# Optimization experiments

Measured on AMD Instinct MI355X. Metric: run time of the kernel, lower is better.

## Reference

```python
import jax, jax.numpy as jnp
import numpy as np

R = 1          # box filter radius -> 3x3 kernel
EPS = 0.01     # regularization


def _box_kernel(r, ch):
    k = 2 * r + 1
    return jnp.full((ch, 1, k, k), 1.0 / (k * k), dtype=jnp.float32)


def _box(x, kernel, groups):
    # depthwise box filter, stride 1, 'same' padding (NCHW)
    return jax.lax.conv_general_dilated(
        x, kernel, window_strides=(1, 1), padding='SAME',
        dimension_numbers=('NCHW', 'OIHW', 'NCHW'),
        feature_group_count=groups)


def setup_inputs() -> dict:
    key = jax.random.key(0)
    k1, k2 = jax.random.split(key)
    shape = (8, 3, 1024, 1024)
    return {
        'x': jax.random.normal(k1, shape, dtype=jnp.float32),
        'y': jax.random.normal(k2, shape, dtype=jnp.float32),
    }


def reference(x, y):
    _, C, H, W = x.shape
    kC = _box_kernel(R, C)   # per-channel depthwise kernel
    k1 = _box_kernel(R, 1)   # normalization kernel
    # N counts valid pixels under 'same' (zero) padding -> edge correction
    Nrm = _box(jnp.ones((1, 1, H, W), x.dtype), k1, 1)
    mean_x = _box(x, kC, C) / Nrm
    mean_y = _box(y, kC, C) / Nrm
    cov_xy = _box(x * y, kC, C) / Nrm - mean_x * mean_y
    var_x = _box(x * x, kC, C) / Nrm - mean_x * mean_x
    A = cov_xy / (var_x + EPS)
    b = mean_y - A * mean_x
    mean_A = _box(A, kC, C) / Nrm
    mean_b = _box(b, kC, C) / Nrm
    return mean_A * x + mean_b
```

## Files before the change

kernel.cpp:

```cpp
#include <hip/hip_runtime.h>


#define H 1024
#define W 1024
#define TILE 32

__global__ __launch_bounds__(256) void guided_filter_kernel(
    const float* __restrict__ x, const float* __restrict__ y,
    float* __restrict__ out)
{
    __shared__ float sx[36][37];
    __shared__ float sy[36][37];
    __shared__ float sA[34][35];
    __shared__ float sB[34][35];

    const int tid = threadIdx.x;
    const int gx0 = blockIdx.x * TILE;
    const int gy0 = blockIdx.y * TILE;
    const long base = (long)blockIdx.z * (long)(H * W);
    const float* __restrict__ xp = x + base;
    const float* __restrict__ yp = y + base;
    float* __restrict__ op = out + base;

    for (int idx = tid; idx < 36 * 36; idx += 256) {
        const int li = idx / 36;
        const int lj = idx - li * 36;
        const int gi = gy0 - 2 + li;
        const int gj = gx0 - 2 + lj;
        float xv = 0.0f, yv = 0.0f;
        if ((unsigned)gi < (unsigned)H && (unsigned)gj < (unsigned)W) {
            const int o = gi * W + gj;
            xv = xp[o];
            yv = yp[o];
        }
        sx[li][lj] = xv;
        sy[li][lj] = yv;
    }
    __syncthreads();

    const float third = 1.0f / 3.0f;

    for (int idx = tid; idx < 34 * 34; idx += 256) {
        const int ai = idx / 34;
        const int aj = idx - ai * 34;
        const int gi = gy0 - 1 + ai;
        const int gj = gx0 - 1 + aj;
        float Av = 0.0f, Bv = 0.0f;
        if ((unsigned)gi < (unsigned)H && (unsigned)gj < (unsigned)W) {
            float sxs = 0.0f, sys = 0.0f, sxx = 0.0f, sxy = 0.0f;
#pragma unroll
            for (int di = 0; di < 3; ++di) {
#pragma unroll
                for (int dj = 0; dj < 3; ++dj) {
                    const float xv = sx[ai + di][aj + dj];
                    const float yv = sy[ai + di][aj + dj];
                    sxs += xv;
                    sys += yv;
                    sxx = fmaf(xv, xv, sxx);
                    sxy = fmaf(xv, yv, sxy);
                }
            }
            const float invr = (gi == 0 || gi == H - 1) ? 0.5f : third;
            const float invc = (gj == 0 || gj == W - 1) ? 0.5f : third;
            const float inv  = invr * invc;
            const float mx = sxs * inv;
            const float my = sys * inv;
            const float cov = fmaf(-mx, my, sxy * inv);
            const float var = fmaf(-mx, mx, sxx * inv);
            Av = cov / (var + 0.01f);
            Bv = fmaf(-Av, mx, my);
        }
        sA[ai][aj] = Av;
        sB[ai][aj] = Bv;
    }
    __syncthreads();

    const int tx = tid & 31;
    const int ty = tid >> 5;
#pragma unroll
    for (int r = 0; r < 4; ++r) {
        const int oi = ty + 8 * r;
        const int oj = tx;
        const int gi = gy0 + oi;
        const int gj = gx0 + oj;
        float sA9 = 0.0f, sB9 = 0.0f;
#pragma unroll
        for (int di = 0; di < 3; ++di) {
#pragma unroll
            for (int dj = 0; dj < 3; ++dj) {
                sA9 += sA[oi + di][oj + dj];
                sB9 += sB[oi + di][oj + dj];
            }
        }
        const float invr = (gi == 0 || gi == H - 1) ? 0.5f : third;
        const float invc = (gj == 0 || gj == W - 1) ? 0.5f : third;
        const float inv  = invr * invc;
        const float mA = sA9 * inv;
        const float mB = sB9 * inv;
        op[gi * W + gj] = fmaf(mA, sx[oi + 2][oj + 2], mB);
    }
}

extern "C" void kernel_launch(void* const* d_in, const int* in_sizes, int n_in,
                              void* d_out, int out_size, void* d_ws, size_t ws_size,
                              hipStream_t stream) {
    const float* x = (const float*)d_in[0];
    const float* y = (const float*)d_in[1];
    float* out = (float*)d_out;
    const int planes = in_sizes[0] / (H * W);
    dim3 grid(W / TILE, H / TILE, planes);
    guided_filter_kernel<<<grid, dim3(256), 0, stream>>>(x, y, out);
}
```

Baseline: 279.9 us.

## Replace shared-memory tiles with register sliding-window wavefront strips using shuffles

Each wavefront now walks down a 32-row strip of a 128-column band. Every lane holds two columns as float2 and keeps rolling 3-row register windows of column partial sums, fetching horizontal neighbours with cross-lane shuffles plus a lane-0/lane-63 halo. This removes LDS staging, the block barriers and the redundant 2-pixel halo recomputation per 32x32 tile. It also prefetches the next row and uses a fast reciprocal in place of division. The cost is higher register pressure, halo loads per strip, and a small precision change from rcp.

```diff
diff --git a/kernel.cpp b/kernel.cpp
--- a/kernel.cpp
+++ b/kernel.cpp
@@ -3,101 +3,175 @@
 
 #define H 1024
 #define W 1024
-#define TILE 32
+#define STRIP 32
+#define WAVES 4
+#define WVC 128
 
-__global__ __launch_bounds__(256) void guided_filter_kernel(
-    const float* __restrict__ x, const float* __restrict__ y,
-    float* __restrict__ out)
+__global__ __launch_bounds__(256, 4) void gf_kernel(const float* __restrict__ xg,
+                                                    const float* __restrict__ yg,
+                                                    float* __restrict__ og)
 {
-    __shared__ float sx[36][37];
-    __shared__ float sy[36][37];
-    __shared__ float sA[34][35];
-    __shared__ float sB[34][35];
+    const int lane = threadIdx.x & 63;
+    const int wv = threadIdx.x >> 6;
+    const int c0 = blockIdx.x * WVC;
+    const int R0 = (blockIdx.y * WAVES + wv) * STRIP;
+    const size_t base = (size_t)blockIdx.z * (size_t)(H * W);
+    const float* __restrict__ xp = xg + base;
+    const float* __restrict__ yp = yg + base;
+    float* __restrict__ op = og + base;
 
-    const int tid = threadIdx.x;
-    const int gx0 = blockIdx.x * TILE;
-    const int gy0 = blockIdx.y * TILE;
-    const long base = (long)blockIdx.z * (long)(H * W);
-    const float* __restrict__ xp = x + base;
-    const float* __restrict__ yp = y + base;
-    float* __restrict__ op = out + base;
-
-    for (int idx = tid; idx < 36 * 36; idx += 256) {
-        const int li = idx / 36;
-        const int lj = idx - li * 36;
-        const int gi = gy0 - 2 + li;
-        const int gj = gx0 - 2 + lj;
-        float xv = 0.0f, yv = 0.0f;
-        if ((unsigned)gi < (unsigned)H && (unsigned)gj < (unsigned)W) {
-            const int o = gi * W + gj;
-            xv = xp[o];
-            yv = yp[o];
-        }
-        sx[li][lj] = xv;
-        sy[li][lj] = yv;
-    }
-    __syncthreads();
+    const int colA = c0 + 2 * lane;
+    const bool isL = (lane == 0);
+    const bool isR = (lane == 63);
+    const bool haloIn = isL ? (c0 > 0) : (isR ? (c0 + WVC < W) : false);
+    const int hdelta = (isL ? (c0 - 2) : (c0 + WVC)) - colA;
 
     const float third = 1.0f / 3.0f;
+    const float invcA = (colA == 0) ? 0.5f : third;
+    const float invcB = (colA + 1 == W - 1) ? 0.5f : third;
+    const float invcH = haloIn ? third : 0.0f;
 
-    for (int idx = tid; idx < 34 * 34; idx += 256) {
-        const int ai = idx / 34;
-        const int aj = idx - ai * 34;
-        const int gi = gy0 - 1 + ai;
-        const int gj = gx0 - 1 + aj;
-        float Av = 0.0f, Bv = 0.0f;
-        if ((unsigned)gi < (unsigned)H && (unsigned)gj < (unsigned)W) {
-            float sxs = 0.0f, sys = 0.0f, sxx = 0.0f, sxy = 0.0f;
-#pragma unroll
-            for (int di = 0; di < 3; ++di) {
-#pragma unroll
-                for (int dj = 0; dj < 3; ++dj) {
-                    const float xv = sx[ai + di][aj + dj];
-                    const float yv = sy[ai + di][aj + dj];
-                    sxs += xv;
-                    sys += yv;
-                    sxx = fmaf(xv, xv, sxx);
-                    sxy = fmaf(xv, yv, sxy);
-                }
-            }
-            const float invr = (gi == 0 || gi == H - 1) ? 0.5f : third;
-            const float invc = (gj == 0 || gj == W - 1) ? 0.5f : third;
-            const float inv  = invr * invc;
-            const float mx = sxs * inv;
-            const float my = sys * inv;
-            const float cov = fmaf(-mx, my, sxy * inv);
-            const float var = fmaf(-mx, mx, sxx * inv);
-            Av = cov / (var + 0.01f);
-            Bv = fmaf(-Av, mx, my);
+    float hxA[3]={0,0,0}, hxB[3]={0,0,0}, hyA[3]={0,0,0}, hyB[3]={0,0,0};
+    float hxxA[3]={0,0,0}, hxxB[3]={0,0,0}, hxyA[3]={0,0,0}, hxyB[3]={0,0,0};
+    float hxH[3]={0,0,0}, hyH[3]={0,0,0}, hxxH[3]={0,0,0}, hxyH[3]={0,0,0};
+    float hAA[3]={0,0,0}, hAB[3]={0,0,0}, hbA[3]={0,0,0}, hbB[3]={0,0,0};
+    float xwA[3]={0,0,0}, xwB[3]={0,0,0};
+
+    int off = (R0 - 2) * W + colA;
+
+    float2 xv = {0,0}, yv = {0,0}, xh = {0,0}, yh = {0,0};
+    if (R0 - 2 >= 0) {
+        xv = *(const float2*)(xp + off);
+        yv = *(const float2*)(yp + off);
+        if (haloIn) {
+            xh = *(const float2*)(xp + off + hdelta);
+            yh = *(const float2*)(yp + off + hdelta);
         }
-        sA[ai][aj] = Av;
-        sB[ai][aj] = Bv;
     }
-    __syncthreads();
 
-    const int tx = tid & 31;
-    const int ty = tid >> 5;
-#pragma unroll
-    for (int r = 0; r < 4; ++r) {
-        const int oi = ty + 8 * r;
-        const int oj = tx;
-        const int gi = gy0 + oi;
-        const int gj = gx0 + oj;
-        float sA9 = 0.0f, sB9 = 0.0f;
-#pragma unroll
-        for (int di = 0; di < 3; ++di) {
-#pragma unroll
-            for (int dj = 0; dj < 3; ++dj) {
-                sA9 += sA[oi + di][oj + dj];
-                sB9 += sB[oi + di][oj + dj];
+#pragma unroll 3
+    for (int s = 0; s < STRIP + 4; ++s) {
+        const int lr = R0 - 2 + s;
+        const int t = lr - 1;
+        const int r = lr - 2;
+
+        const int lrn = lr + 1;
+        float2 xvN = {0,0}, yvN = {0,0}, xhN = {0,0}, yhN = {0,0};
+        if (lrn >= 0 && lrn < H && s < STRIP + 3) {
+            const int offn = off + W;
+            xvN = *(const float2*)(xp + offn);
+            yvN = *(const float2*)(yp + offn);
+            if (haloIn) {
+                xhN = *(const float2*)(xp + offn + hdelta);
+                yhN = *(const float2*)(yp + offn + hdelta);
             }
         }
-        const float invr = (gi == 0 || gi == H - 1) ? 0.5f : third;
-        const float invc = (gj == 0 || gj == W - 1) ? 0.5f : third;
-        const float inv  = invr * invc;
-        const float mA = sA9 * inv;
-        const float mB = sB9 * inv;
-        op[gi * W + gj] = fmaf(mA, sx[oi + 2][oj + 2], mB);
+
+        const float xxA = xv.x * xv.x, xxB = xv.y * xv.y;
+        const float xyA = xv.x * yv.x, xyB = xv.y * yv.y;
+        float xl = __shfl_up(xv.y, 1, 64);
+        float xr = __shfl_down(xv.x, 1, 64);
+        float yl = __shfl_up(yv.y, 1, 64);
+        float yr = __shfl_down(yv.x, 1, 64);
+        xl = isL ? xh.y : xl;
+        xr = isR ? xh.x : xr;
+        yl = isL ? yh.y : yl;
+        yr = isR ? yh.x : yr;
+
+        hxA[0]=hxA[1]; hxA[1]=hxA[2];   hxB[0]=hxB[1]; hxB[1]=hxB[2];
+        hyA[0]=hyA[1]; hyA[1]=hyA[2];   hyB[0]=hyB[1]; hyB[1]=hyB[2];
+        hxxA[0]=hxxA[1]; hxxA[1]=hxxA[2]; hxxB[0]=hxxB[1]; hxxB[1]=hxxB[2];
+        hxyA[0]=hxyA[1]; hxyA[1]=hxyA[2]; hxyB[0]=hxyB[1]; hxyB[1]=hxyB[2];
+        hxH[0]=hxH[1]; hxH[1]=hxH[2];   hyH[0]=hyH[1]; hyH[1]=hyH[2];
+        hxxH[0]=hxxH[1]; hxxH[1]=hxxH[2]; hxyH[0]=hxyH[1]; hxyH[1]=hxyH[2];
+
+        const float sx = xv.x + xv.y;
+        hxA[2] = xl + sx;   hxB[2] = sx + xr;
+        const float sy = yv.x + yv.y;
+        hyA[2] = yl + sy;   hyB[2] = sy + yr;
+        const float sxx = xxA + xxB;
+        hxxA[2] = fmaf(xl, xl, sxx);  hxxB[2] = fmaf(xr, xr, sxx);
+        const float sxy = xyA + xyB;
+        hxyA[2] = fmaf(xl, yl, sxy);  hxyB[2] = fmaf(xr, yr, sxy);
+
+        const float selx  = isL ? xv.x : xv.y;
+        const float sely  = isL ? yv.x : yv.y;
+        const float selxx = isL ? xxA : xxB;
+        const float selxy = isL ? xyA : xyB;
+        hxH[2]  = xh.x + xh.y + selx;
+        hyH[2]  = yh.x + yh.y + sely;
+        hxxH[2] = fmaf(xh.x, xh.x, fmaf(xh.y, xh.y, selxx));
+        hxyH[2] = fmaf(xh.x, yh.x, fmaf(xh.y, yh.y, selxy));
+
+        const float rowfA = (t < 0 || t >= H) ? 0.0f
+                          : ((t == 0 || t == H - 1) ? 0.5f : third);
+        const float iA = rowfA * invcA;
+        const float iB = rowfA * invcB;
+        const float iH = rowfA * invcH;
+
+        float AcA, bcA, AcB, bcB, Ah, bh;
+        {
+            const float mx  = (hxA[0] + hxA[1] + hxA[2]) * iA;
+            const float my  = (hyA[0] + hyA[1] + hyA[2]) * iA;
+            const float mxx = (hxxA[0] + hxxA[1] + hxxA[2]) * iA;
+            const float mxy = (hxyA[0] + hxyA[1] + hxyA[2]) * iA;
+            const float var = fmaf(-mx, mx, mxx);
+            const float cov = fmaf(-mx, my, mxy);
+            AcA = cov * __builtin_amdgcn_rcpf(var + 0.01f);
+            bcA = fmaf(-AcA, mx, my);
+        }
+        {
+            const float mx  = (hxB[0] + hxB[1] + hxB[2]) * iB;
+            const float my  = (hyB[0] + hyB[1] + hyB[2]) * iB;
+            const float mxx = (hxxB[0] + hxxB[1] + hxxB[2]) * iB;
+            const float mxy = (hxyB[0] + hxyB[1] + hxyB[2]) * iB;
+            const float var = fmaf(-mx, mx, mxx);
+            const float cov = fmaf(-mx, my, mxy);
+            AcB = cov * __builtin_amdgcn_rcpf(var + 0.01f);
+            bcB = fmaf(-AcB, mx, my);
+        }
+        {
+            const float mx  = (hxH[0] + hxH[1] + hxH[2]) * iH;
+            const float my  = (hyH[0] + hyH[1] + hyH[2]) * iH;
+            const float mxx = (hxxH[0] + hxxH[1] + hxxH[2]) * iH;
+            const float mxy = (hxyH[0] + hxyH[1] + hxyH[2]) * iH;
+            const float var = fmaf(-mx, mx, mxx);
+            const float cov = fmaf(-mx, my, mxy);
+            Ah = cov * __builtin_amdgcn_rcpf(var + 0.01f);
+            bh = fmaf(-Ah, mx, my);
+        }
+
+        float Al = __shfl_up(AcB, 1, 64);
+        float Ar = __shfl_down(AcA, 1, 64);
+        float bl = __shfl_up(bcB, 1, 64);
+        float br = __shfl_down(bcA, 1, 64);
+        Al = isL ? Ah : Al;   Ar = isR ? Ah : Ar;
+        bl = isL ? bh : bl;   br = isR ? bh : br;
+
+        hAA[0]=hAA[1]; hAA[1]=hAA[2];  hAB[0]=hAB[1]; hAB[1]=hAB[2];
+        hbA[0]=hbA[1]; hbA[1]=hbA[2];  hbB[0]=hbB[1]; hbB[1]=hbB[2];
+        const float sA = AcA + AcB;
+        hAA[2] = Al + sA;  hAB[2] = sA + Ar;
+        const float sb = bcA + bcB;
+        hbA[2] = bl + sb;  hbB[2] = sb + br;
+
+        xwA[0]=xwA[1]; xwA[1]=xwA[2]; xwA[2]=xv.x;
+        xwB[0]=xwB[1]; xwB[1]=xwB[2]; xwB[2]=xv.y;
+
+        if (s >= 4) {
+            const float rowfO = (r == 0 || r == H - 1) ? 0.5f : third;
+            const float oA = rowfO * invcA;
+            const float oB = rowfO * invcB;
+            float2 o;
+            o.x = fmaf((hAA[0] + hAA[1] + hAA[2]) * oA, xwA[0],
+                       (hbA[0] + hbA[1] + hbA[2]) * oA);
+            o.y = fmaf((hAB[0] + hAB[1] + hAB[2]) * oB, xwB[0],
+                       (hbB[0] + hbB[1] + hbB[2]) * oB);
+            *(float2*)(op + (off - 2 * W)) = o;
+        }
+
+        xv = xvN; yv = yvN; xh = xhN; yh = yhN;
+        off += W;
     }
 }
 
@@ -108,6 +182,6 @@
     const float* y = (const float*)d_in[1];
     float* out = (float*)d_out;
     const int planes = in_sizes[0] / (H * W);
-    dim3 grid(W / TILE, H / TILE, planes);
-    guided_filter_kernel<<<grid, dim3(256), 0, stream>>>(x, y, out);
+    dim3 grid(W / WVC, H / (STRIP * WAVES), planes);
+    gf_kernel<<<grid, dim3(256), 0, stream>>>(x, y, out);
 }
```

Measured after the change: 263.2 us. -6.0%, faster.
